# Kernel optimization log

Measured on AMD Instinct MI355X. Metric: run time of the kernel, lower is better.

Reference implementation:

```python
import jax, jax.numpy as jnp
import numpy as np

N = 8192


def setup_inputs() -> dict:
    key = jax.random.key(0)
    k1, k2, k3, k4, k5, k6 = jax.random.split(key, 6)
    return {
        "t": jnp.zeros((1,), dtype=jnp.float32),
        "state": jax.random.uniform(k1, (3 * N,), dtype=jnp.float32),
        "betas": jax.random.uniform(k2, (N,), dtype=jnp.float32),
        "deltas": jax.random.uniform(k3, (N,), dtype=jnp.float32),
        "cs": jax.random.uniform(k4, (N,), dtype=jnp.float32),
        "ps": jax.random.uniform(k5, (N,), dtype=jnp.float32),
        "ts": jax.random.uniform(k6, (N, N), dtype=jnp.float32),
    }


def reference(t, state, betas, deltas, cs, ps, ts):
    # state is interleaved (U_0, I_0, V_0, U_1, I_1, V_1, ...)
    s = state.reshape(N, 3)
    U, I, V = s[:, 0], s[:, 1], s[:, 2]
    # squared_parametrization applied to per-host rate parameters
    beta = jnp.square(betas)
    delta = jnp.square(deltas)
    c = jnp.square(cs)
    p = jnp.square(ps)

    infect = beta * U * V  # (N,)
    dU = -infect
    dI = infect - delta * I
    # neighbor sum over nbr != n of ts[nbr, n] * V[nbr]  ==  ts^T @ V - diag(ts) * V
    coupling = ts.T @ V - jnp.diagonal(ts) * V
    dV = p * I - c * V + coupling

    return jnp.stack([dU, dI, dV], axis=1).reshape(-1)
```

## Files before the change

### kernel.cpp

```cpp
#include <hip/hip_runtime.h>

#define NN 8192

__global__ __launch_bounds__(256) void init_kernel(
    const float* __restrict__ state,
    const float* __restrict__ betas,
    const float* __restrict__ deltas,
    const float* __restrict__ cs,
    const float* __restrict__ ps,
    const float* __restrict__ ts,
    float* __restrict__ out)
{
    int j = blockIdx.x * 256 + threadIdx.x;
    float U = state[3 * j + 0];
    float I = state[3 * j + 1];
    float V = state[3 * j + 2];
    float beta  = betas[j]  * betas[j];
    float delta = deltas[j] * deltas[j];
    float c     = cs[j]     * cs[j];
    float p     = ps[j]     * ps[j];
    float infect = beta * U * V;
    float diag = ts[(size_t)j * NN + j];
    out[3 * j + 0] = -infect;
    out[3 * j + 1] = infect - delta * I;
    out[3 * j + 2] = p * I - c * V - diag * V;
}

__global__ __launch_bounds__(256) void matvec_kernel(
    const float* __restrict__ ts,
    const float* __restrict__ state,
    float* __restrict__ out)
{
    const int colChunk = blockIdx.x & 7;
    const int rowChunk = blockIdx.x >> 3;
    const int j0 = colChunk * 1024 + threadIdx.x * 4;
    const int r0 = rowChunk * 32;

    float v[32];
#pragma unroll
    for (int ii = 0; ii < 32; ++ii)
        v[ii] = state[3 * (r0 + ii) + 2];

    const float* tsp = ts + (size_t)r0 * NN + j0;
    float4 acc = make_float4(0.f, 0.f, 0.f, 0.f);

#pragma unroll 8
    for (int ii = 0; ii < 32; ++ii) {
        float4 t = *(const float4*)(tsp + (size_t)ii * NN);
        acc.x += t.x * v[ii];
        acc.y += t.y * v[ii];
        acc.z += t.z * v[ii];
        acc.w += t.w * v[ii];
    }

    atomicAdd(&out[3 * (j0 + 0) + 2], acc.x);
    atomicAdd(&out[3 * (j0 + 1) + 2], acc.y);
    atomicAdd(&out[3 * (j0 + 2) + 2], acc.z);
    atomicAdd(&out[3 * (j0 + 3) + 2], acc.w);
}

extern "C" void kernel_launch(void* const* d_in, const int* in_sizes, int n_in,
                              void* d_out, int out_size, void* d_ws, size_t ws_size,
                              hipStream_t stream) {
    const float* state  = (const float*)d_in[1];
    const float* betas  = (const float*)d_in[2];
    const float* deltas = (const float*)d_in[3];
    const float* cs     = (const float*)d_in[4];
    const float* ps     = (const float*)d_in[5];
    const float* ts     = (const float*)d_in[6];
    float* out = (float*)d_out;

    init_kernel<<<NN / 256, 256, 0, stream>>>(state, betas, deltas, cs, ps, ts, out);
    matvec_kernel<<<2048, 256, 0, stream>>>(ts, state, out);
}
```

Baseline: 406.1 us.

## Replace atomic matvec reduction with two-stage workspace partial sums

The transposed matvec now runs as 512 blocks, each covering 16 full rows. Each block writes 8192 partial column sums to a workspace buffer. A second kernel reduces the 512 partials per column and fuses the elementwise U/I/V derivative computation, which removes the separate init kernel and all global atomics. The cost is 16 MB of extra workspace traffic and fewer blocks in the main stream over ts.

Measured after the change: 374.8 us. -7.7%, faster.

```diff
diff --git a/kernel.cpp b/kernel.cpp
--- a/kernel.cpp
+++ b/kernel.cpp
@@ -1,8 +1,44 @@
 #include <hip/hip_runtime.h>
 
 #define NN 8192
+#define S1_BLOCKS 512
+#define ROWS_PER_BLOCK (NN / S1_BLOCKS)
 
-__global__ __launch_bounds__(256) void init_kernel(
+__global__ __launch_bounds__(256) void partial_matvec(
+    const float* __restrict__ ts,
+    const float* __restrict__ state,
+    float* __restrict__ ws)
+{
+    const int b = blockIdx.x;
+    const int t = threadIdx.x;
+    const int r0 = b * ROWS_PER_BLOCK;
+
+    float4 acc[8];
+#pragma unroll
+    for (int s = 0; s < 8; ++s) acc[s] = make_float4(0.f, 0.f, 0.f, 0.f);
+
+    const float* base = ts + (size_t)r0 * NN + t * 4;
+    for (int r = 0; r < ROWS_PER_BLOCK; ++r) {
+        float v = state[3 * (r0 + r) + 2];
+        const float* rowp = base + (size_t)r * NN;
+#pragma unroll
+        for (int s = 0; s < 8; ++s) {
+            float4 x = *(const float4*)(rowp + s * 1024);
+            acc[s].x += x.x * v;
+            acc[s].y += x.y * v;
+            acc[s].z += x.z * v;
+            acc[s].w += x.w * v;
+        }
+    }
+
+    float* wsb = ws + (size_t)b * NN + t * 4;
+#pragma unroll
+    for (int s = 0; s < 8; ++s)
+        *(float4*)(wsb + s * 1024) = acc[s];
+}
+
+__global__ __launch_bounds__(256) void finalize_kernel(
+    const float* __restrict__ ws,
     const float* __restrict__ state,
     const float* __restrict__ betas,
     const float* __restrict__ deltas,
@@ -11,52 +47,41 @@
     const float* __restrict__ ts,
     float* __restrict__ out)
 {
-    int j = blockIdx.x * 256 + threadIdx.x;
-    float U = state[3 * j + 0];
-    float I = state[3 * j + 1];
-    float V = state[3 * j + 2];
-    float beta  = betas[j]  * betas[j];
-    float delta = deltas[j] * deltas[j];
-    float c     = cs[j]     * cs[j];
-    float p     = ps[j]     * ps[j];
-    float infect = beta * U * V;
-    float diag = ts[(size_t)j * NN + j];
-    out[3 * j + 0] = -infect;
-    out[3 * j + 1] = infect - delta * I;
-    out[3 * j + 2] = p * I - c * V - diag * V;
-}
+    const int bb = blockIdx.x;
+    const int t  = threadIdx.x;
+    const int cl = t & 31;
+    const int g  = t >> 5;
+    const int col = bb * 32 + cl;
 
-__global__ __launch_bounds__(256) void matvec_kernel(
-    const float* __restrict__ ts,
-    const float* __restrict__ state,
-    float* __restrict__ out)
-{
-    const int colChunk = blockIdx.x & 7;
-    const int rowChunk = blockIdx.x >> 3;
-    const int j0 = colChunk * 1024 + threadIdx.x * 4;
-    const int r0 = rowChunk * 32;
+    float sum = 0.f;
+    const float* p = ws + (size_t)(g * 64) * NN + col;
+#pragma unroll 8
+    for (int k = 0; k < 64; ++k)
+        sum += p[(size_t)k * NN];
 
-    float v[32];
+    __shared__ float red[8][32];
+    red[g][cl] = sum;
+    __syncthreads();
+
+    if (t < 32) {
+        float coupling = 0.f;
 #pragma unroll
-    for (int ii = 0; ii < 32; ++ii)
-        v[ii] = state[3 * (r0 + ii) + 2];
+        for (int g2 = 0; g2 < 8; ++g2) coupling += red[g2][t];
 
-    const float* tsp = ts + (size_t)r0 * NN + j0;
-    float4 acc = make_float4(0.f, 0.f, 0.f, 0.f);
-
-#pragma unroll 8
-    for (int ii = 0; ii < 32; ++ii) {
-        float4 t = *(const float4*)(tsp + (size_t)ii * NN);
-        acc.x += t.x * v[ii];
-        acc.y += t.y * v[ii];
-        acc.z += t.z * v[ii];
-        acc.w += t.w * v[ii];
+        const int j = bb * 32 + t;
+        float U = state[3 * j + 0];
+        float I = state[3 * j + 1];
+        float V = state[3 * j + 2];
+        float beta  = betas[j]  * betas[j];
+        float delta = deltas[j] * deltas[j];
+        float c     = cs[j]     * cs[j];
+        float pp    = ps[j]     * ps[j];
+        float diag  = ts[(size_t)j * NN + j];
+        float infect = beta * U * V;
+        out[3 * j + 0] = -infect;
+        out[3 * j + 1] = infect - delta * I;
+        out[3 * j + 2] = pp * I - c * V - diag * V + coupling;
     }
-
-    atomicAdd(&out[3 * (j0 + 0) + 2], acc.x);
-    atomicAdd(&out[3 * (j0 + 1) + 2], acc.y);
-    atomicAdd(&out[3 * (j0 + 2) + 2], acc.z);
-    atomicAdd(&out[3 * (j0 + 3) + 2], acc.w);
 }
 
 extern "C" void kernel_launch(void* const* d_in, const int* in_sizes, int n_in,
@@ -69,7 +94,9 @@
     const float* ps     = (const float*)d_in[5];
     const float* ts     = (const float*)d_in[6];
     float* out = (float*)d_out;
+    float* ws  = (float*)d_ws;
 
-    init_kernel<<<NN / 256, 256, 0, stream>>>(state, betas, deltas, cs, ps, ts, out);
-    matvec_kernel<<<2048, 256, 0, stream>>>(ts, state, out);
+    partial_matvec<<<S1_BLOCKS, 256, 0, stream>>>(ts, state, ws);
+    finalize_kernel<<<NN / 32, 256, 0, stream>>>(ws, state, betas, deltas,
+                                                 cs, ps, ts, out);
 }
```
